# Kernel tuning notes

Measured on AMD Instinct MI355X. Metric: run time of the kernel, lower is better.

## Reference

```python
import jax, jax.numpy as jnp
import numpy as np

NUM_VECTORS = 8192
DIM = 64

def setup_inputs() -> dict:
    key = jax.random.key(0)
    kx, kw = jax.random.split(key)
    x = jax.random.normal(kx, (8, 4096, DIM), dtype=jnp.float32)
    W = jax.random.normal(kw, (NUM_VECTORS, DIM), dtype=jnp.float32)
    return {"x": x, "W": W}

def reference(x, W):
    # x: [B, S, C] channels_last (ndim==3 -> channels_first=False)
    shape = x.shape
    flat = x.reshape(-1, shape[-1])  # [N, C]
    # cdist + argmin: argmin of squared euclidean distance is identical to argmin of cdist
    x2 = jnp.sum(flat * flat, axis=1, keepdims=True)          # [N, 1]
    w2 = jnp.sum(W * W, axis=1)                                # [K]
    d2 = x2 - 2.0 * (flat @ W.T) + w2                          # [N, K] dominant intermediate
    indices = jnp.argmin(d2, axis=1)                           # [N]
    z = W[indices]                                             # gather [N, C]
    # losses (use_ema=True -> codebook_loss = 0)
    commitment_loss = jnp.mean((z - jax.lax.stop_gradient(flat)) ** 2)
    codebook_loss = jnp.zeros_like(commitment_loss)
    # straight-through estimator
    z_st = flat + jax.lax.stop_gradient(z - flat)
    # perplexity: scatter one-hot counts -> mean -> entropy
    n = flat.shape[0]
    counts = jnp.zeros((NUM_VECTORS,), dtype=jnp.float32).at[indices].add(1.0)
    avg_probs = counts / n
    perplexity = jnp.exp(-jnp.sum(avg_probs * jnp.log(avg_probs + 1e-10)))
    z_out = z_st.reshape(shape)
    return (z_out, codebook_loss, commitment_loss, perplexity)
```

## Files before the change

### kernel.cpp

```cpp
#include <hip/hip_runtime.h>
#include <math.h>

#define N_ROWS 32768
#define K_CODES 8192
#define DIM 64
#define CHUNKS 4
#define CPC (K_CODES / CHUNKS)
#define TILES (CPC / 32)

using half8  = __attribute__((ext_vector_type(8))) _Float16;
using f32x16 = __attribute__((ext_vector_type(16))) float;

#define WS_W2     0
#define WS_COUNTS 32768
#define WS_CSUM   65536
#define WS_ESUM   65540
#define WS_DONE   65544
#define WS_BEST   65552
#define WS_X2     327696
#define WS_WHL    458768

__device__ __forceinline__ void gload_lds16(const _Float16* g, _Float16* l) {
    __builtin_amdgcn_global_load_lds(
        (const __attribute__((address_space(1))) void*)g,
        (__attribute__((address_space(3))) void*)l, 16, 0, 0);
}

__global__ __launch_bounds__(256) void vq_prep(const float* __restrict__ W,
                                               const float* __restrict__ x,
                                               _Float16* __restrict__ whl,
                                               float* __restrict__ w2g,
                                               float* __restrict__ x2g,
                                               unsigned long long* __restrict__ best,
                                               int* __restrict__ counts,
                                               float* __restrict__ scal,
                                               int* __restrict__ done) {
    int g = blockIdx.x * 256 + threadIdx.x;
    int code = g >> 6, k = g & 63;
    float w = W[g];
    _Float16 h  = (_Float16)w;
    _Float16 lo = (_Float16)(w - (float)h);
    whl[(size_t)code * 128 + k]      = h;
    whl[(size_t)code * 128 + 64 + k] = lo;
    float s = w * w;
    #pragma unroll
    for (int off = 32; off; off >>= 1) s += __shfl_down(s, off);
    if (k == 0) w2g[code] = s;
    float4 xv = *(const float4*)(x + (size_t)g * 4);
    float ss = xv.x * xv.x + xv.y * xv.y + xv.z * xv.z + xv.w * xv.w;
    #pragma unroll
    for (int off = 8; off; off >>= 1) ss += __shfl_down(ss, off);
    if ((g & 15) == 0) x2g[g >> 4] = ss;
    if (g < N_ROWS)  best[g] = ~0ULL;
    if (g < K_CODES) counts[g] = 0;
    if (g == 0) { scal[0] = 0.f; scal[1] = 0.f; *done = 0; }
}

__global__ __launch_bounds__(512, 4) void vq_mfma(const float* __restrict__ x,
                                                  const _Float16* __restrict__ whl,
                                                  const float* __restrict__ w2g,
                                                  unsigned long long* __restrict__ best) {
    __shared__ __align__(16) _Float16 lds[2][4096];

    const int t     = threadIdx.x;
    const int wv    = t >> 6;
    const int l     = t & 63;
    const int ln31  = l & 31;
    const int lhalf = l >> 5;
    const int chunk = blockIdx.x & (CHUNKS - 1);
    const int rblk  = blockIdx.x / CHUNKS;
    const int rowb  = rblk * 256 + wv * 32;
    const int cbase = chunk * CPC;

    half8 ahi[4], alo[4];
    {
        const float* xr = x + (size_t)(rowb + ln31) * DIM + lhalf * 8;
        #pragma unroll
        for (int kt = 0; kt < 4; ++kt) {
            float4 a0 = *(const float4*)(xr + kt * 16);
            float4 a1 = *(const float4*)(xr + kt * 16 + 4);
            float fa[8] = {a0.x, a0.y, a0.z, a0.w, a1.x, a1.y, a1.z, a1.w};
            #pragma unroll
            for (int j = 0; j < 8; ++j) {
                _Float16 h = (_Float16)fa[j];
                ahi[kt][j] = h;
                alo[kt][j] = (_Float16)(fa[j] - (float)h);
            }
        }
    }

    const _Float16* srcp = whl + (size_t)(cbase + ln31) * 128
                               + ((wv & 1) * 8 + lhalf + 2 * (wv >> 1)) * 8;
    const int ldsG = wv * 512;

    float bv[16];
    int   bi[16];
    #pragma unroll
    for (int s2 = 0; s2 < 16; ++s2) { bv[s2] = 3.4e38f; bi[s2] = 0; }

    gload_lds16(srcp, &lds[0][0] + ldsG);
    __syncthreads();

    const float* w2p = w2g + cbase + ln31;
    int cur = 0;

    for (int tile = 0; tile < TILES; ++tile) {
        if (tile < TILES - 1)
            gload_lds16(srcp + (size_t)(tile + 1) * 4096,
                        &lds[0][0] + (cur ^ 1) * 4096 + ldsG);
        const float w2v = w2p[tile * 32];
        const _Float16* lb = &lds[0][0] + cur * 4096;

        f32x16 acc = {};
        __builtin_amdgcn_s_setprio(1);
        #pragma unroll
        for (int kt = 0; kt < 4; ++kt) {
            half8 bh = *(const half8*)(lb + ((kt * 2 + 0) * 64 + l) * 8);
            half8 bl = *(const half8*)(lb + ((kt * 2 + 1) * 64 + l) * 8);
            acc = __builtin_amdgcn_mfma_f32_32x32x16_f16(ahi[kt], bh, acc, 0, 0, 0);
            acc = __builtin_amdgcn_mfma_f32_32x32x16_f16(alo[kt], bh, acc, 0, 0, 0);
            acc = __builtin_amdgcn_mfma_f32_32x32x16_f16(ahi[kt], bl, acc, 0, 0, 0);
        }
        __builtin_amdgcn_s_setprio(0);

        const int cc = cbase + tile * 32 + ln31;
        #pragma unroll
        for (int s2 = 0; s2 < 16; ++s2) {
            float sA = fmaf(-2.f, acc[s2], w2v);
            if (sA < bv[s2]) { bv[s2] = sA; bi[s2] = cc; }
        }
        __syncthreads();
        cur ^= 1;
    }

    #pragma unroll
    for (int s2 = 0; s2 < 16; ++s2) {
        unsigned uk = __float_as_uint(bv[s2]);
        uk = (uk >> 31) ? ~uk : (uk | 0x80000000u);
        unsigned long long key = ((unsigned long long)uk << 32) | (unsigned)bi[s2];
        #pragma unroll
        for (int off = 16; off; off >>= 1) {
            unsigned long long o = __shfl_xor(key, off);
            key = (o < key) ? o : key;
        }
        if (ln31 == 0) {
            int rl = (s2 & 3) + 8 * (s2 >> 2) + 4 * lhalf;
            atomicMin(&best[rowb + rl], key);
        }
    }
}

__global__ __launch_bounds__(256) void vq_gather(const float* __restrict__ W,
                                                 const unsigned long long* __restrict__ best,
                                                 const float* __restrict__ x2g,
                                                 float* __restrict__ zout,
                                                 int* __restrict__ counts,
                                                 float* __restrict__ csum) {
    int t   = threadIdx.x;
    int row = blockIdx.x * 64 + (t >> 2);
    int seg = t & 3;
    unsigned long long key = best[row];
    int idx = (int)(key & 0xFFFFFFFFULL);

    const float* wrow = W    + (size_t)idx * DIM + seg * 16;
    float*       zrow = zout + (size_t)row * DIM + seg * 16;
    #pragma unroll
    for (int j = 0; j < 16; j += 4) *(float4*)(zrow + j) = *(const float4*)(wrow + j);

    float local = 0.f;
    if (seg == 0) {
        atomicAdd(&counts[idx], 1);
        unsigned uk = (unsigned)(key >> 32);
        unsigned ob = (uk & 0x80000000u) ? (uk & 0x7FFFFFFFu) : ~uk;
        local = x2g[row] + __uint_as_float(ob);
    }
    #pragma unroll
    for (int off = 32; off; off >>= 1) local += __shfl_down(local, off);
    if ((t & 63) == 0) atomicAdd(csum, local);
}

__global__ __launch_bounds__(256) void vq_final(const int* __restrict__ counts,
                                                float* __restrict__ scal,
                                                int* __restrict__ done,
                                                float* __restrict__ out3) {
    __shared__ float sh[4];
    int g = blockIdx.x * 256 + threadIdx.x;
    float p = (float)counts[g] * (1.0f / N_ROWS);
    float e = p * logf(p + 1e-10f);
    #pragma unroll
    for (int off = 32; off; off >>= 1) e += __shfl_down(e, off);
    if ((threadIdx.x & 63) == 0) sh[threadIdx.x >> 6] = e;
    __syncthreads();
    if (threadIdx.x == 0) {
        atomicAdd(&scal[1], sh[0] + sh[1] + sh[2] + sh[3]);
        __threadfence();
        int old = atomicAdd(done, 1);
        if (old == 31) {
            float es = atomicAdd(&scal[1], 0.f);
            float cs = atomicAdd(&scal[0], 0.f);
            out3[0] = 0.f;
            out3[1] = cs * (1.0f / ((float)N_ROWS * DIM));
            out3[2] = expf(-es);
        }
    }
}

extern "C" void kernel_launch(void* const* d_in, const int* in_sizes, int n_in,
                              void* d_out, int out_size, void* d_ws, size_t ws_size,
                              hipStream_t stream) {
    (void)in_sizes; (void)n_in; (void)out_size; (void)ws_size;
    const float* x = (const float*)d_in[0];
    const float* W = (const float*)d_in[1];
    float* zout = (float*)d_out;
    float* out3 = (float*)d_out + (size_t)N_ROWS * DIM;

    float*              w2g    = (float*)((char*)d_ws + WS_W2);
    int*                counts = (int*)((char*)d_ws + WS_COUNTS);
    float*              scal   = (float*)((char*)d_ws + WS_CSUM);
    int*                done   = (int*)((char*)d_ws + WS_DONE);
    unsigned long long* best   = (unsigned long long*)((char*)d_ws + WS_BEST);
    float*              x2g    = (float*)((char*)d_ws + WS_X2);
    _Float16*           whl    = (_Float16*)((char*)d_ws + WS_WHL);

    vq_prep  <<<K_CODES * DIM / 256,     256, 0, stream>>>(W, x, whl, w2g, x2g, best, counts, scal, done);
    vq_mfma  <<<(N_ROWS / 256) * CHUNKS, 512, 0, stream>>>(x, whl, w2g, best);
    vq_gather<<<N_ROWS / 64,             256, 0, stream>>>(W, best, x2g, zout, counts, &scal[0]);
    vq_final <<<K_CODES / 256,           256, 0, stream>>>(counts, scal, done, out3);
}
```

Baseline: 139.0 us.

## Fuse gather and final reduction into one kernel, drop x2 precompute, double chunks

```diff
diff --git a/kernel.cpp b/kernel.cpp
--- a/kernel.cpp
+++ b/kernel.cpp
@@ -4,9 +4,10 @@
 #define N_ROWS 32768
 #define K_CODES 8192
 #define DIM 64
-#define CHUNKS 4
+#define CHUNKS 8
 #define CPC (K_CODES / CHUNKS)
 #define TILES (CPC / 32)
+#define POST_BLOCKS (N_ROWS / 64)
 
 using half8  = __attribute__((ext_vector_type(8))) _Float16;
 using f32x16 = __attribute__((ext_vector_type(16))) float;
@@ -14,11 +15,9 @@
 #define WS_W2     0
 #define WS_COUNTS 32768
 #define WS_CSUM   65536
-#define WS_ESUM   65540
-#define WS_DONE   65544
+#define WS_DONE   65540
 #define WS_BEST   65552
-#define WS_X2     327696
-#define WS_WHL    458768
+#define WS_WHL    327696
 
 __device__ __forceinline__ void gload_lds16(const _Float16* g, _Float16* l) {
     __builtin_amdgcn_global_load_lds(
@@ -27,13 +26,11 @@
 }
 
 __global__ __launch_bounds__(256) void vq_prep(const float* __restrict__ W,
-                                               const float* __restrict__ x,
                                                _Float16* __restrict__ whl,
                                                float* __restrict__ w2g,
-                                               float* __restrict__ x2g,
                                                unsigned long long* __restrict__ best,
                                                int* __restrict__ counts,
-                                               float* __restrict__ scal,
+                                               float* __restrict__ csum,
                                                int* __restrict__ done) {
     int g = blockIdx.x * 256 + threadIdx.x;
     int code = g >> 6, k = g & 63;
@@ -46,14 +43,9 @@
     #pragma unroll
     for (int off = 32; off; off >>= 1) s += __shfl_down(s, off);
     if (k == 0) w2g[code] = s;
-    float4 xv = *(const float4*)(x + (size_t)g * 4);
-    float ss = xv.x * xv.x + xv.y * xv.y + xv.z * xv.z + xv.w * xv.w;
-    #pragma unroll
-    for (int off = 8; off; off >>= 1) ss += __shfl_down(ss, off);
-    if ((g & 15) == 0) x2g[g >> 4] = ss;
     if (g < N_ROWS)  best[g] = ~0ULL;
     if (g < K_CODES) counts[g] = 0;
-    if (g == 0) { scal[0] = 0.f; scal[1] = 0.f; *done = 0; }
+    if (g == 0) { *csum = 0.f; *done = 0; }
 }
 
 __global__ __launch_bounds__(512, 4) void vq_mfma(const float* __restrict__ x,
@@ -150,57 +142,60 @@
     }
 }
 
-__global__ __launch_bounds__(256) void vq_gather(const float* __restrict__ W,
-                                                 const unsigned long long* __restrict__ best,
-                                                 const float* __restrict__ x2g,
-                                                 float* __restrict__ zout,
-                                                 int* __restrict__ counts,
-                                                 float* __restrict__ csum) {
+__global__ __launch_bounds__(256) void vq_post(const float* __restrict__ W,
+                                               const float* __restrict__ x,
+                                               const unsigned long long* __restrict__ best,
+                                               float* __restrict__ zout,
+                                               int* __restrict__ counts,
+                                               float* __restrict__ csum,
+                                               int* __restrict__ done,
+                                               float* __restrict__ out3) {
+    __shared__ float sh[4];
+    __shared__ int sh_done;
     int t   = threadIdx.x;
     int row = blockIdx.x * 64 + (t >> 2);
     int seg = t & 3;
     unsigned long long key = best[row];
     int idx = (int)(key & 0xFFFFFFFFULL);
+    if (seg == 0) atomicAdd(&counts[idx], 1);
 
     const float* wrow = W    + (size_t)idx * DIM + seg * 16;
+    const float* xrow = x    + (size_t)row * DIM + seg * 16;
     float*       zrow = zout + (size_t)row * DIM + seg * 16;
-    #pragma unroll
-    for (int j = 0; j < 16; j += 4) *(float4*)(zrow + j) = *(const float4*)(wrow + j);
-
     float local = 0.f;
-    if (seg == 0) {
-        atomicAdd(&counts[idx], 1);
-        unsigned uk = (unsigned)(key >> 32);
-        unsigned ob = (uk & 0x80000000u) ? (uk & 0x7FFFFFFFu) : ~uk;
-        local = x2g[row] + __uint_as_float(ob);
+    #pragma unroll
+    for (int j = 0; j < 16; j += 4) {
+        float4 wv = *(const float4*)(wrow + j);
+        float4 xv = *(const float4*)(xrow + j);
+        *(float4*)(zrow + j) = wv;
+        float dx = wv.x - xv.x, dy = wv.y - xv.y, dz = wv.z - xv.z, dw = wv.w - xv.w;
+        local += dx * dx + dy * dy + dz * dz + dw * dw;
     }
     #pragma unroll
     for (int off = 32; off; off >>= 1) local += __shfl_down(local, off);
     if ((t & 63) == 0) atomicAdd(csum, local);
-}
-
-__global__ __launch_bounds__(256) void vq_final(const int* __restrict__ counts,
-                                                float* __restrict__ scal,
-                                                int* __restrict__ done,
-                                                float* __restrict__ out3) {
-    __shared__ float sh[4];
-    int g = blockIdx.x * 256 + threadIdx.x;
-    float p = (float)counts[g] * (1.0f / N_ROWS);
-    float e = p * logf(p + 1e-10f);
-    #pragma unroll
-    for (int off = 32; off; off >>= 1) e += __shfl_down(e, off);
-    if ((threadIdx.x & 63) == 0) sh[threadIdx.x >> 6] = e;
+
+    __threadfence();
     __syncthreads();
-    if (threadIdx.x == 0) {
-        atomicAdd(&scal[1], sh[0] + sh[1] + sh[2] + sh[3]);
-        __threadfence();
-        int old = atomicAdd(done, 1);
-        if (old == 31) {
-            float es = atomicAdd(&scal[1], 0.f);
-            float cs = atomicAdd(&scal[0], 0.f);
+    if (t == 0) sh_done = atomicAdd(done, 1);
+    __syncthreads();
+    if (sh_done == POST_BLOCKS - 1) {
+        float e = 0.f;
+        for (int i = t; i < K_CODES; i += 256) {
+            float c = (float)atomicAdd(&counts[i], 0);
+            float p = c * (1.0f / N_ROWS);
+            e += p * logf(p + 1e-10f);
+        }
+        #pragma unroll
+        for (int off = 32; off; off >>= 1) e += __shfl_down(e, off);
+        if ((t & 63) == 0) sh[t >> 6] = e;
+        __syncthreads();
+        if (t == 0) {
+            float etot = sh[0] + sh[1] + sh[2] + sh[3];
+            float cs   = atomicAdd(csum, 0.f);
             out3[0] = 0.f;
             out3[1] = cs * (1.0f / ((float)N_ROWS * DIM));
-            out3[2] = expf(-es);
+            out3[2] = expf(-etot);
         }
     }
 }
@@ -216,14 +211,12 @@
 
     float*              w2g    = (float*)((char*)d_ws + WS_W2);
     int*                counts = (int*)((char*)d_ws + WS_COUNTS);
-    float*              scal   = (float*)((char*)d_ws + WS_CSUM);
+    float*              csum   = (float*)((char*)d_ws + WS_CSUM);
     int*                done   = (int*)((char*)d_ws + WS_DONE);
     unsigned long long* best   = (unsigned long long*)((char*)d_ws + WS_BEST);
-    float*              x2g    = (float*)((char*)d_ws + WS_X2);
     _Float16*           whl    = (_Float16*)((char*)d_ws + WS_WHL);
 
-    vq_prep  <<<K_CODES * DIM / 256,     256, 0, stream>>>(W, x, whl, w2g, x2g, best, counts, scal, done);
-    vq_mfma  <<<(N_ROWS / 256) * CHUNKS, 512, 0, stream>>>(x, whl, w2g, best);
-    vq_gather<<<N_ROWS / 64,             256, 0, stream>>>(W, best, x2g, zout, counts, &scal[0]);
-    vq_final <<<K_CODES / 256,           256, 0, stream>>>(counts, scal, done, out3);
-}
+    vq_prep<<<K_CODES * DIM / 256,       256, 0, stream>>>(W, whl, w2g, best, counts, csum, done);
+    vq_mfma<<<(N_ROWS / 256) * CHUNKS,   512, 0, stream>>>(x, whl, w2g, best);
+    vq_post<<<POST_BLOCKS,               256, 0, stream>>>(W, x, best, zout, counts, csum, done, out3);
+}
```

After: 198.3 us. 1.43x slower.

## Process two codebook tiles per iteration with four-deep LDS buffering

Applied to the files above, without the earlier changes.

```diff
diff --git a/kernel.cpp b/kernel.cpp
--- a/kernel.cpp
+++ b/kernel.cpp
@@ -7,6 +7,7 @@
 #define CHUNKS 4
 #define CPC (K_CODES / CHUNKS)
 #define TILES (CPC / 32)
+#define ITERS (TILES / 2)
 
 using half8  = __attribute__((ext_vector_type(8))) _Float16;
 using f32x16 = __attribute__((ext_vector_type(16))) float;
@@ -60,7 +61,7 @@
                                                   const _Float16* __restrict__ whl,
                                                   const float* __restrict__ w2g,
                                                   unsigned long long* __restrict__ best) {
-    __shared__ __align__(16) _Float16 lds[2][4096];
+    __shared__ __align__(16) _Float16 lds[4][4096];
 
     const int t     = threadIdx.x;
     const int wv    = t >> 6;
@@ -98,39 +99,50 @@
     #pragma unroll
     for (int s2 = 0; s2 < 16; ++s2) { bv[s2] = 3.4e38f; bi[s2] = 0; }
 
-    gload_lds16(srcp, &lds[0][0] + ldsG);
+    gload_lds16(srcp,        &lds[0][0] + ldsG);
+    gload_lds16(srcp + 4096, &lds[1][0] + ldsG);
     __syncthreads();
 
     const float* w2p = w2g + cbase + ln31;
-    int cur = 0;
-
-    for (int tile = 0; tile < TILES; ++tile) {
-        if (tile < TILES - 1)
-            gload_lds16(srcp + (size_t)(tile + 1) * 4096,
-                        &lds[0][0] + (cur ^ 1) * 4096 + ldsG);
-        const float w2v = w2p[tile * 32];
-        const _Float16* lb = &lds[0][0] + cur * 4096;
-
-        f32x16 acc = {};
+
+    for (int it = 0; it < ITERS; ++it) {
+        const int tA = 2 * it, tB = 2 * it + 1;
+        if (it < ITERS - 1) {
+            gload_lds16(srcp + (size_t)(tA + 2) * 4096, &lds[(tA + 2) & 3][0] + ldsG);
+            gload_lds16(srcp + (size_t)(tB + 2) * 4096, &lds[(tB + 2) & 3][0] + ldsG);
+        }
+        const float w2A = w2p[tA * 32];
+        const float w2B = w2p[tB * 32];
+        const _Float16* lbA = &lds[tA & 3][0];
+        const _Float16* lbB = &lds[tB & 3][0];
+
+        f32x16 accA = {}, accB = {};
         __builtin_amdgcn_s_setprio(1);
         #pragma unroll
         for (int kt = 0; kt < 4; ++kt) {
-            half8 bh = *(const half8*)(lb + ((kt * 2 + 0) * 64 + l) * 8);
-            half8 bl = *(const half8*)(lb + ((kt * 2 + 1) * 64 + l) * 8);
-            acc = __builtin_amdgcn_mfma_f32_32x32x16_f16(ahi[kt], bh, acc, 0, 0, 0);
-            acc = __builtin_amdgcn_mfma_f32_32x32x16_f16(alo[kt], bh, acc, 0, 0, 0);
-            acc = __builtin_amdgcn_mfma_f32_32x32x16_f16(ahi[kt], bl, acc, 0, 0, 0);
+            half8 bhA = *(const half8*)(lbA + ((kt * 2 + 0) * 64 + l) * 8);
+            half8 blA = *(const half8*)(lbA + ((kt * 2 + 1) * 64 + l) * 8);
+            half8 bhB = *(const half8*)(lbB + ((kt * 2 + 0) * 64 + l) * 8);
+            half8 blB = *(const half8*)(lbB + ((kt * 2 + 1) * 64 + l) * 8);
+            accA = __builtin_amdgcn_mfma_f32_32x32x16_f16(ahi[kt], bhA, accA, 0, 0, 0);
+            accB = __builtin_amdgcn_mfma_f32_32x32x16_f16(ahi[kt], bhB, accB, 0, 0, 0);
+            accA = __builtin_amdgcn_mfma_f32_32x32x16_f16(alo[kt], bhA, accA, 0, 0, 0);
+            accB = __builtin_amdgcn_mfma_f32_32x32x16_f16(alo[kt], bhB, accB, 0, 0, 0);
+            accA = __builtin_amdgcn_mfma_f32_32x32x16_f16(ahi[kt], blA, accA, 0, 0, 0);
+            accB = __builtin_amdgcn_mfma_f32_32x32x16_f16(ahi[kt], blB, accB, 0, 0, 0);
         }
         __builtin_amdgcn_s_setprio(0);
 
-        const int cc = cbase + tile * 32 + ln31;
+        const int ccA = cbase + tA * 32 + ln31;
+        const int ccB = cbase + tB * 32 + ln31;
         #pragma unroll
         for (int s2 = 0; s2 < 16; ++s2) {
-            float sA = fmaf(-2.f, acc[s2], w2v);
-            if (sA < bv[s2]) { bv[s2] = sA; bi[s2] = cc; }
+            float sA = fmaf(-2.f, accA[s2], w2A);
+            float sB = fmaf(-2.f, accB[s2], w2B);
+            if (sA < bv[s2]) { bv[s2] = sA; bi[s2] = ccA; }
+            if (sB < bv[s2]) { bv[s2] = sB; bi[s2] = ccB; }
         }
         __syncthreads();
-        cur ^= 1;
     }
 
     #pragma unroll
```

New measurement: 138.4 us. About the same (-0.4%).
